# Kernel optimization log

Measured on AMD Instinct MI355X. Metric: run time of the kernel, lower is better.

The kernel has to match this reference:

```python
import jax, jax.numpy as jnp
import numpy as np

B, T, C = 2, 2048, 1024
NH, LAT, DHR = 16, 512, 64
DK = C // NH  # 64


def _rope(x, d):
    # interleaved RoPE as in source: freq = t+1, theta per pair repeated twice
    Tx = x.shape[1]
    freq = jnp.arange(Tx, dtype=jnp.float32)[:, None] + 1.0            # [T,1]
    pos = jnp.arange(d // 2, dtype=jnp.float32)[:, None]
    pos = jnp.repeat(pos, 2, axis=-1).reshape(1, -1)                   # [1,d] -> p0,p0,p1,p1,...
    theta = jnp.exp(-2.0 * pos / d * jnp.log(10000.0))
    cos = jnp.cos(freq * theta)                                        # [T,d]
    sin = jnp.sin(freq * theta)
    x32 = x.astype(jnp.float32)
    x1 = x32[..., 0::2]
    x2 = x32[..., 1::2]
    xrot = jnp.stack([-x2, x1], axis=-1).reshape(x32.shape)
    return (x32 * cos + xrot * sin).astype(x.dtype)


def setup_inputs() -> dict:
    key = jax.random.key(0)
    ks = jax.random.split(key, 13)
    s = lambda k, sh, fan: jax.random.normal(k, sh, jnp.float32) / np.sqrt(fan)
    return {
        'x': jax.random.normal(ks[0], (B, T, C), jnp.float32),
        'w1': s(ks[1], (C, 2 * LAT), C), 'b1': jnp.zeros((2 * LAT,), jnp.float32),
        'wkr': s(ks[2], (2 * LAT, DHR), 2 * LAT), 'bkr': jnp.zeros((DHR,), jnp.float32),
        'wqr': s(ks[3], (2 * LAT, DHR * NH), 2 * LAT), 'bqr': jnp.zeros((DHR * NH,), jnp.float32),
        'wkv': s(ks[4], (LAT, 2 * C), LAT), 'bkv': jnp.zeros((2 * C,), jnp.float32),
        'wq': s(ks[5], (LAT, C), LAT), 'bq': jnp.zeros((C,), jnp.float32),
        'wo': s(ks[6], (C, C), C), 'bo': jnp.zeros((C,), jnp.float32),
    }


def reference(x, w1, b1, wkr, bkr, wqr, bqr, wkv, bkv, wq, bq, wo, bo):
    h = x @ w1 + b1                           # [B,T,2*LAT]
    cKV, cq = jnp.split(h, 2, axis=-1)        # each [B,T,LAT]

    kRt = _rope(h @ wkr + bkr, DHR)           # [B,T,DHR]
    qRt = _rope(h @ wqr + bqr, DHR * NH)      # [B,T,NH*DHR]
    qRt = qRt.reshape(B, T, NH, DHR).transpose(0, 2, 1, 3)  # [B,NH,T,DHR]

    kv = cKV @ wkv + bkv                      # [B,T,2C]
    k, v = jnp.split(kv, 2, axis=-1)
    q = cq @ wq + bq                          # [B,T,C]

    to_heads = lambda t: t.reshape(B, T, NH, DK).transpose(0, 2, 1, 3)
    q, k, v = to_heads(q), to_heads(k), to_heads(v)   # [B,NH,T,DK]

    q = jnp.concatenate([q, qRt], axis=-1)                              # [B,NH,T,DK+DHR]
    kR = jnp.broadcast_to(kRt[:, None, :, :], (B, NH, T, DHR))
    k = jnp.concatenate([k, kR], axis=-1)                               # [B,NH,T,DK+DHR]

    dk = q.shape[-1]
    qf, kf, vf = q.astype(jnp.float32), k.astype(jnp.float32), v.astype(jnp.float32)
    w = jnp.einsum('bnTd,bntd->bnTt', qf, kf) * dk ** (-0.5)            # [B,NH,T,T]
    mask = jnp.tril(jnp.ones((T, T), jnp.float32))
    w = jnp.where(mask == 0, -jnp.inf, w)
    w = jax.nn.softmax(w, axis=-1)
    out = jnp.einsum('bnTt,bntd->bnTd', w, vf).astype(x.dtype)          # [B,NH,T,DK]

    out = out.transpose(0, 2, 1, 3).reshape(B, T, C)
    return out @ wo + bo
```

## Files before the change

### kernel.cpp

```cpp
#include <hip/hip_runtime.h>
#include <math.h>
#include <stdint.h>

#define B_   2
#define T_   2048
#define C_   1024
#define NH_  16
#define LAT_ 512
#define DHR_ 64
#define M_   (B_*T_)

typedef unsigned short u16;
typedef short short8 __attribute__((ext_vector_type(8)));
typedef short short4v __attribute__((ext_vector_type(4)));
typedef float f32x4 __attribute__((ext_vector_type(4)));

#define SCALE2 0.12752455489626498f

__device__ __forceinline__ u16 f2bf(float f) {
    union { float f; unsigned u; } x; x.f = f;
    unsigned r = x.u + 0x7fffu + ((x.u >> 16) & 1u);
    return (u16)(r >> 16);
}
__device__ __forceinline__ u16 f2bf_fast(float f) {
    union { float f; unsigned u; } x; x.f = f;
    return (u16)((x.u + 0x8000u) >> 16);
}
__device__ __forceinline__ float bf2f(u16 v) {
    union { unsigned u; float f; } x; x.u = ((unsigned)v) << 16;
    return x.f;
}

__device__ __forceinline__ void gl_lds16(const void* g, void* l) {
    auto* gp = reinterpret_cast<const __attribute__((address_space(1))) unsigned*>(
        reinterpret_cast<uintptr_t>(g));
    auto* lp = reinterpret_cast<__attribute__((address_space(3))) unsigned*>(
        reinterpret_cast<uintptr_t>(l));
    __builtin_amdgcn_global_load_lds(gp, lp, 16, 0, 0);
}

__device__ __forceinline__ void tr_tile(const float* __restrict__ W,
                                        u16* __restrict__ Wt,
                                        int K, int N, int bx, int by, int tid,
                                        float (*t)[33])
{
    const int tx = tid & 31;
    const int ty = tid >> 5;
    const int n0 = bx << 5;
    const int k0 = by << 5;
    #pragma unroll
    for (int r = 0; r < 4; ++r) {
        int row = ty + (r << 3);
        t[row][tx] = W[(size_t)(k0 + row) * N + n0 + tx];
    }
    __syncthreads();
    #pragma unroll
    for (int r = 0; r < 4; ++r) {
        int row = ty + (r << 3);
        Wt[(size_t)(n0 + row) * K + k0 + tx] = f2bf(t[tx][row]);
    }
}

__global__ __launch_bounds__(256)
void prep_all(const float* __restrict__ x, u16* __restrict__ xb,
              const float* __restrict__ w1,  const float* __restrict__ wqr,
              const float* __restrict__ wkr, const float* __restrict__ wkv,
              const float* __restrict__ wq,  const float* __restrict__ wo,
              u16* __restrict__ w1t,  u16* __restrict__ wqkt,
              u16* __restrict__ wkvt, u16* __restrict__ wqt,
              u16* __restrict__ wot,
              const float* __restrict__ bqr, const float* __restrict__ bkr,
              float* __restrict__ bqk)
{
    __shared__ float t[32][33];
    int id = blockIdx.x;
    const int tid = threadIdx.x;
    if (id < 4096) {
        int i = id * 256 + tid;
        float4 v = ((const float4*)x)[i];
        short4v s;
        s[0] = f2bf(v.x); s[1] = f2bf(v.y); s[2] = f2bf(v.z); s[3] = f2bf(v.w);
        ((short4v*)xb)[i] = s;
        return;
    }
    id -= 4096;
    if (id < 1024)      { tr_tile(w1,  w1t,  1024, 1024, id % 32, id / 32, tid, t); return; }
    id -= 1024;
    if (id < 1024)      { tr_tile(wqr, wqkt, 1024, 1024, id % 32, id / 32, tid, t); return; }
    id -= 1024;
    if (id < 64)        { tr_tile(wkr, wqkt + 1024 * 1024, 1024, 64, id % 2, id / 2, tid, t); return; }
    id -= 64;
    if (id < 1024)      { tr_tile(wkv, wkvt, 512, 2048, id % 64, id / 64, tid, t); return; }
    id -= 1024;
    if (id < 512)       { tr_tile(wq,  wqt,  512, 1024, id % 32, id / 32, tid, t); return; }
    id -= 512;
    if (id < 1024)      { tr_tile(wo,  wot,  1024, 1024, id % 32, id / 32, tid, t); return; }
    for (int i = tid; i < 1152; i += 256) {
        float v;
        if (i < 1024)      v = bqr[i];
        else if (i < 1088) v = bkr[i - 1024];
        else               v = 0.f;
        bqk[i] = v;
    }
}

template<int BM, int BN>
__device__ __forceinline__ void gemm_body(
    u16* __restrict__ AsB, u16* __restrict__ BsB,
    const u16* __restrict__ A, int lda,
    const u16* __restrict__ Bt, const float* __restrict__ bias,
    void* __restrict__ Out, bool outf32, float oscale,
    int N, int K, int m0, int n0, int tid)
{
    constexpr int MI = BM / 32;
    constexpr int NI = BN / 32;
    const int lane = tid & 63;
    const int ln   = lane & 15;
    const int quad = lane >> 4;
    const int wv   = tid >> 6;
    const int wm   = (wv & 1) * (BM / 2);
    const int wn   = (wv >> 1) * (BN / 2);

    f32x4 acc[MI][NI];
    #pragma unroll
    for (int i = 0; i < MI; ++i)
        #pragma unroll
        for (int j = 0; j < NI; ++j) acc[i][j] = (f32x4){0.f, 0.f, 0.f, 0.f};

    auto stage = [&](int bufi, int k0) {
        u16* As = AsB + bufi * (BM * 32);
        u16* Bs = BsB + bufi * (BN * 32);
        #pragma unroll
        for (int it = 0; it < BM / 64; ++it) {
            int flat = it * 256 + tid;
            gl_lds16(A + (size_t)(m0 + (flat >> 2)) * lda + k0 + ((flat & 3) << 3),
                     &As[flat * 8]);
        }
        #pragma unroll
        for (int it = 0; it < BN / 64; ++it) {
            int flat = it * 256 + tid;
            gl_lds16(Bt + (size_t)(n0 + (flat >> 2)) * K + k0 + ((flat & 3) << 3),
                     &Bs[flat * 8]);
        }
    };

    stage(0, 0);
    __syncthreads();

    int buf = 0;
    for (int k0 = 0; k0 < K; k0 += 32) {
        if (k0 + 32 < K) stage(buf ^ 1, k0 + 32);

        u16* As = AsB + buf * (BM * 32);
        u16* Bs = BsB + buf * (BN * 32);
        short8 af[MI], bfv[NI];
        #pragma unroll
        for (int mi = 0; mi < MI; ++mi)
            af[mi] = *(const short8*)(&As[(wm + mi * 16 + ln) * 32 + quad * 8]);
        #pragma unroll
        for (int ni = 0; ni < NI; ++ni)
            bfv[ni] = *(const short8*)(&Bs[(wn + ni * 16 + ln) * 32 + quad * 8]);
        #pragma unroll
        for (int mi = 0; mi < MI; ++mi)
            #pragma unroll
            for (int ni = 0; ni < NI; ++ni)
                acc[mi][ni] = __builtin_amdgcn_mfma_f32_16x16x32_bf16(af[mi], bfv[ni], acc[mi][ni], 0, 0, 0);

        __syncthreads();
        buf ^= 1;
    }

    float bb[NI];
    #pragma unroll
    for (int ni = 0; ni < NI; ++ni) bb[ni] = bias[n0 + wn + ni * 16 + ln];

    #pragma unroll
    for (int mi = 0; mi < MI; ++mi) {
        #pragma unroll
        for (int r = 0; r < 4; ++r) {
            const size_t row = (size_t)(m0 + wm + mi * 16 + quad * 4 + r);
            #pragma unroll
            for (int ni = 0; ni < NI; ++ni) {
                float v = (acc[mi][ni][r] + bb[ni]) * oscale;
                const size_t idx = row * N + n0 + wn + ni * 16 + ln;
                if (outf32) ((float*)Out)[idx] = v;
                else        ((u16*)Out)[idx]  = f2bf(v);
            }
        }
    }
}

template<int BM, int BN, bool OUTF32>
__global__ __launch_bounds__(256, 2)
void gemm_mfma(const u16* __restrict__ A, int lda,
               const u16* __restrict__ Bt,
               const float* __restrict__ bias,
               void* __restrict__ Out, int N, int K, float oscale)
{
    __shared__ __align__(16) u16 As[2 * BM * 32];
    __shared__ __align__(16) u16 Bs[2 * BN * 32];
    gemm_body<BM, BN>(As, Bs, A, lda, Bt, bias, Out, OUTF32, oscale,
                      N, K, blockIdx.y * BM, blockIdx.x * BN, threadIdx.x);
}

__global__ __launch_bounds__(256, 2)
void gemm3(const u16* __restrict__ hb,
           const u16* __restrict__ wqkt, const float* __restrict__ bqk, u16* __restrict__ Zqk,
           const u16* __restrict__ wkvt, const float* __restrict__ bkv, u16* __restrict__ kvbb,
           const u16* __restrict__ wqt,  const float* __restrict__ bq,  u16* __restrict__ qb)
{
    __shared__ __align__(16) u16 As[2 * 4096];
    __shared__ __align__(16) u16 Bs[2 * 4096];
    int id = blockIdx.x;
    const u16* A; const u16* Bt; const float* bias; u16* Out; int N, K, bx, by;
    float osc = 1.0f;
    if (id < 288)      { A = hb;       Bt = wqkt; bias = bqk; Out = Zqk;  N = 1152; K = 1024; bx = id % 9;  by = id / 9; }
    else if (id < 800) { id -= 288; A = hb;       Bt = wkvt; bias = bkv; Out = kvbb; N = 2048; K = 512;  bx = id % 16; by = id / 16; }
    else               { id -= 800; A = hb + 512; Bt = wqt;  bias = bq;  Out = qb;   N = 1024; K = 512;  bx = id % 8;  by = id / 8; osc = SCALE2; }
    gemm_body<128, 128>(As, Bs, A, 1024, Bt, bias, Out, false, osc, N, K,
                        by * 128, bx * 128, threadIdx.x);
}

__global__ void rope_bf(u16* __restrict__ Zqk)
{
    int idx = blockIdx.x * 256 + threadIdx.x;
    u16* p;
    int t;
    float e, osc;
    if (idx < M_ * 512) {
        int row = idx >> 9, pr = idx & 511;
        e = (-2.0f * (float)pr / 1024.0f) * 9.210340371976184f;
        p = Zqk + (size_t)row * 1152 + (pr << 1);
        t = row & (T_ - 1);
        osc = SCALE2;
    } else {
        int r = idx - M_ * 512;
        if (r >= M_ * 32) return;
        int row = r >> 5, pr = r & 31;
        e = (-2.0f * (float)pr / 64.0f) * 9.210340371976184f;
        p = Zqk + 1024 + (size_t)row * 1152 + (pr << 1);
        t = row & (T_ - 1);
        osc = 1.0f;
    }
    float theta = expf(e);
    float ang = (float)(t + 1) * theta;
    float s = sinf(ang), c = cosf(ang);
    float x1 = bf2f(p[0]);
    float x2 = bf2f(p[1]);
    p[0] = f2bf((x1 * c - x2 * s) * osc);
    p[1] = f2bf((x2 * c + x1 * s) * osc);
}

#define KROW  136
#define VROW  72
#define PROW  72

__global__ __launch_bounds__(256, 2)
void attn_mfma(const u16* __restrict__ qh,
               const u16* __restrict__ qR, int qRstride,
               const u16* __restrict__ kv,
               const u16* __restrict__ kR, int kRstride,
               float* __restrict__ Opart,
               float* __restrict__ MLpart)
{
    __shared__ __align__(16) u16 Ks[2][64 * KROW];
    __shared__ __align__(16) u16 Vt[2][64 * VROW];
    __shared__ __align__(16) u16 Ps[4 * 32 * PROW];

    const int tid  = threadIdx.x;
    const int lane = tid & 63;
    const int ln   = lane & 15;
    const int quad = lane >> 4;
    const int wv   = tid >> 6;
    const int bh   = blockIdx.y;
    const int b    = bh >> 4;
    const int h    = bh & 15;
    const int bT   = b * T_;
    const int p    = blockIdx.x & 7;
    const int s    = blockIdx.x >> 3;

    short8 kreg[4];
    u16    vreg[2][8];

    auto prefetch = [&](int kt) {
        const int kbase = bT + (kt << 6);
        #pragma unroll
        for (int it = 0; it < 4; ++it) {
            int flat = tid + (it << 8);
            int j    = flat >> 4;
            int c8   = (flat & 15) << 3;
            const u16* src = (c8 < 64)
                ? (kv + (size_t)(kbase + j) * (2 * C_) + h * 64 + c8)
                : (kR + (size_t)(kbase + j) * kRstride + (c8 - 64));
            kreg[it] = *(const short8*)src;
        }
        #pragma unroll
        for (int it = 0; it < 2; ++it) {
            int flat = tid + (it << 8);
            int dv   = flat & 63;
            int kg   = flat >> 6;
            const u16* vs = kv + (size_t)(kbase + kg * 8) * (2 * C_) + C_ + h * 64 + dv;
            #pragma unroll
            for (int j = 0; j < 8; ++j) vreg[it][j] = vs[(size_t)j * (2 * C_)];
        }
    };
    auto lds_write = [&](int bufi) {
        #pragma unroll
        for (int it = 0; it < 4; ++it) {
            int flat = tid + (it << 8);
            int j    = flat >> 4;
            int c8   = (flat & 15) << 3;
            *(short8*)(&Ks[bufi][j * KROW + c8]) = kreg[it];
        }
        #pragma unroll
        for (int it = 0; it < 2; ++it) {
            int flat = tid + (it << 8);
            int dv   = flat & 63;
            int kg   = flat >> 6;
            short8 vv;
            #pragma unroll
            for (int j = 0; j < 8; ++j) vv[j] = (short)vreg[it][j];
            *(short8*)(&Vt[bufi][dv * VROW + kg * 8]) = vv;
        }
    };

    const int qts[2]    = { p, 15 - p };
    const int halves[2] = { s, 1 - s };

    for (int seg = 0; seg < 2; ++seg) {
        const int qt   = qts[seg];
        const int hf   = halves[seg];
        const int n    = 2 * qt + 2;
        const int ktlo = hf ? (n >> 1) : 0;
        const int kthi = hf ? n : (n >> 1);
        const int part = ((bh * 16 + qt) << 1) + hf;
        const int wq0  = qt * 128 + wv * 32;

        short8 aq[2][4];
        #pragma unroll
        for (int ni = 0; ni < 2; ++ni) {
            const size_t row = (size_t)(bT + wq0 + ni * 16 + ln);
            #pragma unroll
            for (int kk = 0; kk < 4; ++kk) {
                const int col = kk * 32 + quad * 8;
                const u16* src = (kk < 2)
                    ? (qh + row * C_ + h * 64 + col)
                    : (qR + row * qRstride + h * 64 + (col - 64));
                aq[ni][kk] = *(const short8*)src;
            }
        }

        f32x4 O[2][4];
        float m_run[2], l_run[2];
        #pragma unroll
        for (int ni = 0; ni < 2; ++ni) {
            m_run[ni] = -1e30f;
            l_run[ni] = 0.f;
            #pragma unroll
            for (int mt = 0; mt < 4; ++mt) O[ni][mt] = (f32x4){0.f, 0.f, 0.f, 0.f};
        }

        prefetch(ktlo);
        lds_write(0);
        if (ktlo + 1 < kthi) prefetch(ktlo + 1);
        __syncthreads();

        for (int kt = ktlo; kt < kthi; ++kt) {
            const int cur = (kt - ktlo) & 1;
            if (kt + 1 < kthi) lds_write(cur ^ 1);
            if (kt + 2 < kthi) prefetch(kt + 2);

            const int k0 = kt << 6;
            if (k0 <= wq0 + 31) {
                f32x4 S[2][4];
                #pragma unroll
                for (int ni = 0; ni < 2; ++ni)
                    #pragma unroll
                    for (int mi = 0; mi < 4; ++mi)
                        S[ni][mi] = (f32x4){0.f, 0.f, 0.f, 0.f};

                #pragma unroll
                for (int kk = 0; kk < 4; ++kk) {
                    #pragma unroll
                    for (int mi = 0; mi < 4; ++mi) {
                        short8 ak = *(const short8*)(&Ks[cur][(mi * 16 + ln) * KROW + kk * 32 + quad * 8]);
                        S[0][mi] = __builtin_amdgcn_mfma_f32_16x16x32_bf16(ak, aq[0][kk], S[0][mi], 0, 0, 0);
                        S[1][mi] = __builtin_amdgcn_mfma_f32_16x16x32_bf16(ak, aq[1][kk], S[1][mi], 0, 0, 0);
                    }
                }

                const bool full = (k0 + 63) <= wq0;

                #pragma unroll
                for (int ni = 0; ni < 2; ++ni) {
                    const int qg = wq0 + ni * 16 + ln;
                    float sv[16];
                    float mloc = -1e30f;
                    #pragma unroll
                    for (int mi = 0; mi < 4; ++mi)
                        #pragma unroll
                        for (int r = 0; r < 4; ++r) {
                            float sc = S[ni][mi][r];
                            if (!full) {
                                int key = k0 + mi * 16 + quad * 4 + r;
                                if (key > qg) sc = -1e30f;
                            }
                            sv[mi * 4 + r] = sc;
                            mloc = fmaxf(mloc, sc);
                        }
                    mloc = fmaxf(mloc, __shfl_xor(mloc, 16));
                    mloc = fmaxf(mloc, __shfl_xor(mloc, 32));
                    const float mold  = m_run[ni];
                    const float mnew  = fmaxf(mold, mloc);
                    const float alpha = exp2f(mold - mnew);
                    m_run[ni] = mnew;

                    float lsum = 0.f;
                    #pragma unroll
                    for (int mi = 0; mi < 4; ++mi) {
                        float p0 = exp2f(sv[mi * 4 + 0] - mnew);
                        float p1 = exp2f(sv[mi * 4 + 1] - mnew);
                        float p2 = exp2f(sv[mi * 4 + 2] - mnew);
                        float p3 = exp2f(sv[mi * 4 + 3] - mnew);
                        lsum += (p0 + p1) + (p2 + p3);
                        short4v pk;
                        pk[0] = (short)f2bf_fast(p0); pk[1] = (short)f2bf_fast(p1);
                        pk[2] = (short)f2bf_fast(p2); pk[3] = (short)f2bf_fast(p3);
                        *(short4v*)(&Ps[(wv * 32 + ni * 16 + ln) * PROW + mi * 16 + quad * 4]) = pk;
                    }
                    lsum += __shfl_xor(lsum, 16);
                    lsum += __shfl_xor(lsum, 32);
                    l_run[ni] = l_run[ni] * alpha + lsum;

                    #pragma unroll
                    for (int mt = 0; mt < 4; ++mt) {
                        O[ni][mt][0] *= alpha;
                        O[ni][mt][1] *= alpha;
                        O[ni][mt][2] *= alpha;
                        O[ni][mt][3] *= alpha;
                    }
                }

                asm volatile("s_waitcnt lgkmcnt(0)" ::: "memory");

                #pragma unroll
                for (int c = 0; c < 2; ++c) {
                    short8 pb0 = *(const short8*)(&Ps[(wv * 32 +  0 + ln) * PROW + c * 32 + quad * 8]);
                    short8 pb1 = *(const short8*)(&Ps[(wv * 32 + 16 + ln) * PROW + c * 32 + quad * 8]);
                    #pragma unroll
                    for (int mt = 0; mt < 4; ++mt) {
                        short8 av = *(const short8*)(&Vt[cur][(mt * 16 + ln) * VROW + c * 32 + quad * 8]);
                        O[0][mt] = __builtin_amdgcn_mfma_f32_16x16x32_bf16(av, pb0, O[0][mt], 0, 0, 0);
                        O[1][mt] = __builtin_amdgcn_mfma_f32_16x16x32_bf16(av, pb1, O[1][mt], 0, 0, 0);
                    }
                }
            }
            __syncthreads();
        }

        #pragma unroll
        for (int ni = 0; ni < 2; ++ni) {
            const int qlocal = wv * 32 + ni * 16 + ln;
            float* dst = Opart + ((size_t)part * 128 + qlocal) * 64;
            #pragma unroll
            for (int mt = 0; mt < 4; ++mt)
                *(f32x4*)(dst + mt * 16 + quad * 4) = O[ni][mt];
            if (quad == 0) {
                float2* ml = (float2*)MLpart;
                ml[part * 128 + qlocal] = make_float2(m_run[ni], l_run[ni]);
            }
        }
    }
}

__global__ void attn_merge(const float* __restrict__ Opart,
                           const float* __restrict__ MLpart,
                           u16* __restrict__ out)
{
    int g = blockIdx.x * 256 + threadIdx.x;
    int row    = g >> 4;
    int c4     = (g & 15) << 2;
    int bhqt   = row >> 7;
    int qlocal = row & 127;
    const float2* ml = (const float2*)MLpart;
    float2 ml0 = ml[(bhqt << 1) * 128 + qlocal];
    float2 ml1 = ml[((bhqt << 1) + 1) * 128 + qlocal];
    float m  = fmaxf(ml0.x, ml1.x);
    float a0 = exp2f(ml0.x - m);
    float a1 = exp2f(ml1.x - m);
    float inv = 1.0f / (ml0.y * a0 + ml1.y * a1);
    const float4 o0 = *(const float4*)(Opart + ((size_t)(bhqt << 1) * 128 + qlocal) * 64 + c4);
    const float4 o1 = *(const float4*)(Opart + ((size_t)((bhqt << 1) + 1) * 128 + qlocal) * 64 + c4);
    int bh = bhqt >> 4, qt = bhqt & 15;
    int b = bh >> 4, h = bh & 15;
    size_t orow = (size_t)(b * T_ + qt * 128 + qlocal);
    short4v o;
    o[0] = (short)f2bf((o0.x * a0 + o1.x * a1) * inv);
    o[1] = (short)f2bf((o0.y * a0 + o1.y * a1) * inv);
    o[2] = (short)f2bf((o0.z * a0 + o1.z * a1) * inv);
    o[3] = (short)f2bf((o0.w * a0 + o1.w * a1) * inv);
    *(short4v*)(out + orow * C_ + h * 64 + c4) = o;
}

extern "C" void kernel_launch(void* const* d_in, const int* in_sizes, int n_in,
                              void* d_out, int out_size, void* d_ws, size_t ws_size,
                              hipStream_t stream)
{
    const float* x   = (const float*)d_in[0];
    const float* w1  = (const float*)d_in[1];
    const float* b1  = (const float*)d_in[2];
    const float* wkr = (const float*)d_in[3];
    const float* bkr = (const float*)d_in[4];
    const float* wqr = (const float*)d_in[5];
    const float* bqr = (const float*)d_in[6];
    const float* wkv = (const float*)d_in[7];
    const float* bkv = (const float*)d_in[8];
    const float* wq  = (const float*)d_in[9];
    const float* bq  = (const float*)d_in[10];
    const float* wo  = (const float*)d_in[11];
    const float* bo  = (const float*)d_in[12];
    float* out = (float*)d_out;

    u16* ws    = (u16*)d_ws;
    u16* buf0  = ws;
    u16* buf1  = buf0 + 4194304;
    u16* Zqk   = buf1 + 4194304;
    u16* kvbb  = Zqk  + 4718592;
    u16* w1t   = kvbb + 8388608;
    u16* wqkt  = w1t  + 1048576;
    u16* wkvt  = wqkt + 1179648;
    u16* wqt   = wkvt + 1048576;
    u16* wot   = wqt  + 524288;
    float* bqk   = (float*)(wot + 1048576);
    float* Opart = bqk + 1280;
    float* MLprt = Opart + 8388608;

    u16* xb    = buf0;
    u16* qb    = buf0;
    u16* hb    = buf1;
    u16* attnb = buf1;

    dim3 blk(256);

    prep_all<<<8769, blk, 0, stream>>>(x, xb, w1, wqr, wkr, wkv, wq, wo,
                                       w1t, wqkt, wkvt, wqt, wot,
                                       bqr, bkr, bqk);

    gemm_mfma<128, 64, false><<<dim3(16, 32), blk, 0, stream>>>(xb, 1024, w1t, b1, hb, 1024, 1024, 1.0f);
    gemm3<<<1056, blk, 0, stream>>>(hb, wqkt, bqk, Zqk, wkvt, bkv, kvbb, wqt, bq, qb);
    rope_bf<<<(M_ * 544 + 255) / 256, blk, 0, stream>>>(Zqk);
    attn_mfma<<<dim3(16, 32), blk, 0, stream>>>(qb, Zqk, 1152, kvbb, Zqk + 1024, 1152, Opart, MLprt);
    attn_merge<<<4096, blk, 0, stream>>>(Opart, MLprt, attnb);
    gemm_mfma<128, 64, true><<<dim3(16, 32), blk, 0, stream>>>(attnb, 1024, wot, bo, out, 1024, 1024, 1.0f);
}
```

Baseline: 251.3 us.

## Pre-swizzle K/V into per-head layouts and stage via direct global-to-LDS loads

Adds a reshape_kv kernel that copies K (with the shared rope key) and a transposed V into contiguous per-head buffers using an XOR swizzle. The attention kernel then stages tiles with gl_lds16 direct global-to-LDS copies instead of a register prefetch plus strided scalar V gathers, and uses XOR-swizzled unpadded LDS layouts for K, V and P to avoid bank conflicts. Partial outputs are stored as bf16 instead of fp32 to halve merge traffic. This costs an extra kernel launch and a round trip of about 24 MB through global memory, and rounding partial outputs to bf16 loses some precision.

```diff
diff --git a/kernel.cpp b/kernel.cpp
--- a/kernel.cpp
+++ b/kernel.cpp
@@ -251,21 +251,64 @@
     p[1] = f2bf((x2 * c + x1 * s) * osc);
 }
 
-#define KROW  136
-#define VROW  72
-#define PROW  72
+__global__ __launch_bounds__(256)
+void reshape_kv(const u16* __restrict__ kvb,
+                const u16* __restrict__ kR, int kRstride,
+                u16* __restrict__ Kf,
+                u16* __restrict__ Vt)
+{
+    __shared__ u16 t[64 * 68];
+    const int tid = threadIdx.x;
+    const int bh  = blockIdx.y;
+    const int kt  = blockIdx.x;
+    const int b = bh >> 4, h = bh & 15;
+    const int bT = b * T_;
+    const int k0 = kt << 6;
+
+    #pragma unroll
+    for (int it = 0; it < 4; ++it) {
+        int flat = it * 256 + tid;
+        int j = flat >> 4;
+        int g = flat & 15;
+        int gl = g ^ (j & 7);
+        const u16* src = (g < 8)
+            ? (kvb + (size_t)(bT + k0 + j) * 2048 + h * 64 + ((gl & 7) << 3))
+            : (kR  + (size_t)(bT + k0 + j) * kRstride + ((gl & 7) << 3));
+        *(short8*)(Kf + ((size_t)bh * 2048 + k0 + j) * 128 + (g << 3)) = *(const short8*)src;
+    }
+    #pragma unroll
+    for (int it = 0; it < 2; ++it) {
+        int flat = it * 256 + tid;
+        int j  = flat >> 3;
+        int d8 = (flat & 7) << 3;
+        *(short8*)(&t[j * 68 + d8]) =
+            *(const short8*)(kvb + (size_t)(bT + k0 + j) * 2048 + 1024 + h * 64 + d8);
+    }
+    __syncthreads();
+    #pragma unroll
+    for (int it = 0; it < 2; ++it) {
+        int flat = it * 256 + tid;
+        int dv = flat >> 3;
+        int p  = flat & 7;
+        int gl = p ^ (dv & 7);
+        short8 v;
+        #pragma unroll
+        for (int e = 0; e < 8; ++e) v[e] = (short)t[(gl * 8 + e) * 68 + dv];
+        *(short8*)(Vt + (size_t)bh * 131072 + (size_t)dv * 2048 + k0 + (p << 3)) = v;
+    }
+}
 
 __global__ __launch_bounds__(256, 2)
 void attn_mfma(const u16* __restrict__ qh,
                const u16* __restrict__ qR, int qRstride,
-               const u16* __restrict__ kv,
-               const u16* __restrict__ kR, int kRstride,
-               float* __restrict__ Opart,
+               const u16* __restrict__ Kf,
+               const u16* __restrict__ Vtg,
+               u16* __restrict__ Opart,
                float* __restrict__ MLpart)
 {
-    __shared__ __align__(16) u16 Ks[2][64 * KROW];
-    __shared__ __align__(16) u16 Vt[2][64 * VROW];
-    __shared__ __align__(16) u16 Ps[4 * 32 * PROW];
+    __shared__ __align__(16) u16 Ks[2][64 * 128];
+    __shared__ __align__(16) u16 Vt[2][64 * 64];
+    __shared__ __align__(16) u16 Ps[4 * 32 * 64];
 
     const int tid  = threadIdx.x;
     const int lane = tid & 63;
@@ -278,49 +321,21 @@
     const int bT   = b * T_;
     const int p    = blockIdx.x & 7;
     const int s    = blockIdx.x >> 3;
-
-    short8 kreg[4];
-    u16    vreg[2][8];
-
-    auto prefetch = [&](int kt) {
-        const int kbase = bT + (kt << 6);
+    const int ln7  = ln & 7;
+
+    auto stage = [&](int bufi, int kt) {
+        const u16* ksrc = Kf + ((size_t)bh * 2048 + (kt << 6)) * 128;
         #pragma unroll
         for (int it = 0; it < 4; ++it) {
-            int flat = tid + (it << 8);
-            int j    = flat >> 4;
-            int c8   = (flat & 15) << 3;
-            const u16* src = (c8 < 64)
-                ? (kv + (size_t)(kbase + j) * (2 * C_) + h * 64 + c8)
-                : (kR + (size_t)(kbase + j) * kRstride + (c8 - 64));
-            kreg[it] = *(const short8*)src;
-        }
+            int flat = it * 256 + tid;
+            gl_lds16(ksrc + flat * 8, &Ks[bufi][flat * 8]);
+        }
+        const u16* vsrc = Vtg + (size_t)bh * 131072 + (kt << 6);
         #pragma unroll
         for (int it = 0; it < 2; ++it) {
-            int flat = tid + (it << 8);
-            int dv   = flat & 63;
-            int kg   = flat >> 6;
-            const u16* vs = kv + (size_t)(kbase + kg * 8) * (2 * C_) + C_ + h * 64 + dv;
-            #pragma unroll
-            for (int j = 0; j < 8; ++j) vreg[it][j] = vs[(size_t)j * (2 * C_)];
-        }
-    };
-    auto lds_write = [&](int bufi) {
-        #pragma unroll
-        for (int it = 0; it < 4; ++it) {
-            int flat = tid + (it << 8);
-            int j    = flat >> 4;
-            int c8   = (flat & 15) << 3;
-            *(short8*)(&Ks[bufi][j * KROW + c8]) = kreg[it];
-        }
-        #pragma unroll
-        for (int it = 0; it < 2; ++it) {
-            int flat = tid + (it << 8);
-            int dv   = flat & 63;
-            int kg   = flat >> 6;
-            short8 vv;
-            #pragma unroll
-            for (int j = 0; j < 8; ++j) vv[j] = (short)vreg[it][j];
-            *(short8*)(&Vt[bufi][dv * VROW + kg * 8]) = vv;
+            int flat = it * 256 + tid;
+            gl_lds16(vsrc + (size_t)(flat >> 3) * 2048 + ((flat & 7) << 3),
+                     &Vt[bufi][flat * 8]);
         }
     };
 
@@ -360,15 +375,12 @@
             for (int mt = 0; mt < 4; ++mt) O[ni][mt] = (f32x4){0.f, 0.f, 0.f, 0.f};
         }
 
-        prefetch(ktlo);
-        lds_write(0);
-        if (ktlo + 1 < kthi) prefetch(ktlo + 1);
+        stage(0, ktlo);
         __syncthreads();
 
         for (int kt = ktlo; kt < kthi; ++kt) {
             const int cur = (kt - ktlo) & 1;
-            if (kt + 1 < kthi) lds_write(cur ^ 1);
-            if (kt + 2 < kthi) prefetch(kt + 2);
+            if (kt + 1 < kthi) stage(cur ^ 1, kt + 1);
 
             const int k0 = kt << 6;
             if (k0 <= wq0 + 31) {
@@ -383,7 +395,8 @@
                 for (int kk = 0; kk < 4; ++kk) {
                     #pragma unroll
                     for (int mi = 0; mi < 4; ++mi) {
-                        short8 ak = *(const short8*)(&Ks[cur][(mi * 16 + ln) * KROW + kk * 32 + quad * 8]);
+                        short8 ak = *(const short8*)(
+                            &Ks[cur][(mi * 16 + ln) * 128 + (((kk * 4 + quad) ^ ln7) << 3)]);
                         S[0][mi] = __builtin_amdgcn_mfma_f32_16x16x32_bf16(ak, aq[0][kk], S[0][mi], 0, 0, 0);
                         S[1][mi] = __builtin_amdgcn_mfma_f32_16x16x32_bf16(ak, aq[1][kk], S[1][mi], 0, 0, 0);
                     }
@@ -426,7 +439,9 @@
                         short4v pk;
                         pk[0] = (short)f2bf_fast(p0); pk[1] = (short)f2bf_fast(p1);
                         pk[2] = (short)f2bf_fast(p2); pk[3] = (short)f2bf_fast(p3);
-                        *(short4v*)(&Ps[(wv * 32 + ni * 16 + ln) * PROW + mi * 16 + quad * 4]) = pk;
+                        *(short4v*)(&Ps[(wv * 32 + ni * 16 + ln) * 64 +
+                                        (((mi * 2 + (quad >> 1)) ^ ln7) << 3) +
+                                        ((quad & 1) << 2)]) = pk;
                     }
                     lsum += __shfl_xor(lsum, 16);
                     lsum += __shfl_xor(lsum, 32);
@@ -445,11 +460,12 @@
 
                 #pragma unroll
                 for (int c = 0; c < 2; ++c) {
-                    short8 pb0 = *(const short8*)(&Ps[(wv * 32 +  0 + ln) * PROW + c * 32 + quad * 8]);
-                    short8 pb1 = *(const short8*)(&Ps[(wv * 32 + 16 + ln) * PROW + c * 32 + quad * 8]);
+                    const int pos = ((c * 4 + quad) ^ ln7) << 3;
+                    short8 pb0 = *(const short8*)(&Ps[(wv * 32 +  0 + ln) * 64 + pos]);
+                    short8 pb1 = *(const short8*)(&Ps[(wv * 32 + 16 + ln) * 64 + pos]);
                     #pragma unroll
                     for (int mt = 0; mt < 4; ++mt) {
-                        short8 av = *(const short8*)(&Vt[cur][(mt * 16 + ln) * VROW + c * 32 + quad * 8]);
+                        short8 av = *(const short8*)(&Vt[cur][(mt * 16 + ln) * 64 + pos]);
                         O[0][mt] = __builtin_amdgcn_mfma_f32_16x16x32_bf16(av, pb0, O[0][mt], 0, 0, 0);
                         O[1][mt] = __builtin_amdgcn_mfma_f32_16x16x32_bf16(av, pb1, O[1][mt], 0, 0, 0);
                     }
@@ -461,10 +477,16 @@
         #pragma unroll
         for (int ni = 0; ni < 2; ++ni) {
             const int qlocal = wv * 32 + ni * 16 + ln;
-            float* dst = Opart + ((size_t)part * 128 + qlocal) * 64;
+            u16* dst = Opart + ((size_t)part * 128 + qlocal) * 64;
             #pragma unroll
-            for (int mt = 0; mt < 4; ++mt)
-                *(f32x4*)(dst + mt * 16 + quad * 4) = O[ni][mt];
+            for (int mt = 0; mt < 4; ++mt) {
+                short4v o;
+                o[0] = (short)f2bf(O[ni][mt][0]);
+                o[1] = (short)f2bf(O[ni][mt][1]);
+                o[2] = (short)f2bf(O[ni][mt][2]);
+                o[3] = (short)f2bf(O[ni][mt][3]);
+                *(short4v*)(dst + mt * 16 + quad * 4) = o;
+            }
             if (quad == 0) {
                 float2* ml = (float2*)MLpart;
                 ml[part * 128 + qlocal] = make_float2(m_run[ni], l_run[ni]);
@@ -473,7 +495,7 @@
     }
 }
 
-__global__ void attn_merge(const float* __restrict__ Opart,
+__global__ void attn_merge(const u16* __restrict__ Opart,
                            const float* __restrict__ MLpart,
                            u16* __restrict__ out)
 {
@@ -489,16 +511,18 @@
     float a0 = exp2f(ml0.x - m);
     float a1 = exp2f(ml1.x - m);
     float inv = 1.0f / (ml0.y * a0 + ml1.y * a1);
-    const float4 o0 = *(const float4*)(Opart + ((size_t)(bhqt << 1) * 128 + qlocal) * 64 + c4);
-    const float4 o1 = *(const float4*)(Opart + ((size_t)((bhqt << 1) + 1) * 128 + qlocal) * 64 + c4);
+    const u16* o0p = Opart + ((size_t)(bhqt << 1) * 128 + qlocal) * 64 + c4;
+    const u16* o1p = Opart + ((size_t)((bhqt << 1) + 1) * 128 + qlocal) * 64 + c4;
+    short4v s0 = *(const short4v*)o0p;
+    short4v s1 = *(const short4v*)o1p;
     int bh = bhqt >> 4, qt = bhqt & 15;
     int b = bh >> 4, h = bh & 15;
     size_t orow = (size_t)(b * T_ + qt * 128 + qlocal);
     short4v o;
-    o[0] = (short)f2bf((o0.x * a0 + o1.x * a1) * inv);
-    o[1] = (short)f2bf((o0.y * a0 + o1.y * a1) * inv);
-    o[2] = (short)f2bf((o0.z * a0 + o1.z * a1) * inv);
-    o[3] = (short)f2bf((o0.w * a0 + o1.w * a1) * inv);
+    o[0] = (short)f2bf((bf2f((u16)s0[0]) * a0 + bf2f((u16)s1[0]) * a1) * inv);
+    o[1] = (short)f2bf((bf2f((u16)s0[1]) * a0 + bf2f((u16)s1[1]) * a1) * inv);
+    o[2] = (short)f2bf((bf2f((u16)s0[2]) * a0 + bf2f((u16)s1[2]) * a1) * inv);
+    o[3] = (short)f2bf((bf2f((u16)s0[3]) * a0 + bf2f((u16)s1[3]) * a1) * inv);
     *(short4v*)(out + orow * C_ + h * 64 + c4) = o;
 }
 
@@ -531,9 +555,11 @@
     u16* wkvt  = wqkt + 1179648;
     u16* wqt   = wkvt + 1048576;
     u16* wot   = wqt  + 524288;
-    float* bqk   = (float*)(wot + 1048576);
-    float* Opart = bqk + 1280;
-    float* MLprt = Opart + 8388608;
+    float* bqk = (float*)(wot + 1048576);
+    u16* Kf    = (u16*)(bqk + 1280);
+    u16* Vtg   = Kf  + 8388608;
+    u16* Opart = Vtg + 4194304;
+    float* MLprt = (float*)(Opart + 8388608);
 
     u16* xb    = buf0;
     u16* qb    = buf0;
@@ -549,7 +575,8 @@
     gemm_mfma<128, 64, false><<<dim3(16, 32), blk, 0, stream>>>(xb, 1024, w1t, b1, hb, 1024, 1024, 1.0f);
     gemm3<<<1056, blk, 0, stream>>>(hb, wqkt, bqk, Zqk, wkvt, bkv, kvbb, wqt, bq, qb);
     rope_bf<<<(M_ * 544 + 255) / 256, blk, 0, stream>>>(Zqk);
-    attn_mfma<<<dim3(16, 32), blk, 0, stream>>>(qb, Zqk, 1152, kvbb, Zqk + 1024, 1152, Opart, MLprt);
+    reshape_kv<<<dim3(32, 32), blk, 0, stream>>>(kvbb, Zqk + 1024, 1152, Kf, Vtg);
+    attn_mfma<<<dim3(16, 32), blk, 0, stream>>>(qb, Zqk, 1152, Kf, Vtg, Opart, MLprt);
     attn_merge<<<4096, blk, 0, stream>>>(Opart, MLprt, attnb);
     gemm_mfma<128, 64, true><<<dim3(16, 32), blk, 0, stream>>>(attnb, 1024, wot, bo, out, 1024, 1024, 1.0f);
 }
```

Measured after the change: 251.9 us. Within noise of the previous version (+0.2%).
